# Kernel tuning notes

Measured on AMD Instinct MI355X. Metric: run time of the kernel, lower is better.

## Reference

```python
import jax, jax.numpy as jnp
import numpy as np
from jax import lax

B, L, N_INP, N_HID = 128, 128, 1, 2048
DT = 0.042
RHO = 0.99
INPUT_SCALING = 1.0
GAMMA_MIN, GAMMA_MAX = 2.0, 3.0
EPS_MIN, EPS_MAX = 4.0, 5.0
THETA = 0.1
ALPHA, BETA, TAU_REF = 0.3, 0.4, 0.25  # bio_cell constants


def setup_inputs() -> dict:
    rng = np.random.default_rng(0)
    x = jnp.asarray(rng.standard_normal((B, L, N_INP)), dtype=jnp.float32)
    # per-neuron gamma / epsilon drawn uniformly from (min, max) as in __init__
    gamma = jnp.asarray(rng.uniform(GAMMA_MIN, GAMMA_MAX, N_HID), dtype=jnp.float32)
    epsilon = jnp.asarray(rng.uniform(EPS_MIN, EPS_MAX, N_HID), dtype=jnp.float32)
    # h2h = 2 * (2*rand - 1), then spectral-norm scaled to radius rho
    h2h_np = 2.0 * (2.0 * rng.random((N_HID, N_HID)) - 1.0)
    eig_max = np.abs(np.linalg.eigvals(h2h_np)).max()
    h2h = jnp.asarray(h2h_np * (RHO / eig_max), dtype=jnp.float32)
    x2h = jnp.asarray(rng.random((N_INP, N_HID)) * INPUT_SCALING, dtype=jnp.float32)
    bias = jnp.asarray((rng.random(N_HID) * 2.0 - 1.0) * INPUT_SCALING, dtype=jnp.float32)
    return {"x": x, "h2h": h2h, "x2h": x2h, "bias": bias, "gamma": gamma, "epsilon": epsilon}


def reference(x, h2h, x2h, bias, gamma, epsilon):
    # bio_cell recurrence over L steps; returns mean spike rates (B, N_HID)
    dt = jnp.float32(DT)
    ref_decay = jnp.exp(jnp.float32(-DT / TAU_REF))

    def step(carry, xt):
        hy, hz, ref = carry  # each (B, N_HID); xt: (B, N_INP)
        pre = jnp.tanh(xt @ x2h + hy @ h2h + bias)
        hz = hz + dt * (pre - gamma * hy - epsilon * hz)
        hy = hy + dt * hz
        s = (hy - THETA - ref > 0).astype(hy.dtype)  # spike (non-diff)
        hy = hy * (1.0 - s * ALPHA)
        hz = hz * (1.0 - s * BETA)
        ref = ref * ref_decay + s
        return (hy, hz, ref), s

    z = jnp.zeros((x.shape[0], h2h.shape[0]), x.dtype)
    _, spikes = lax.scan(step, (z, z, z), jnp.swapaxes(x, 0, 1))  # spikes: (L, B, N_HID)
    return spikes.mean(axis=0)
```

## Files before the change

### kernel.cpp

```cpp
#include <hip/hip_runtime.h>
#include <hip/hip_bf16.h>
#include <cmath>

constexpr int   BB  = 128;
constexpr int   LL  = 128;
constexpr int   NH  = 2048;
constexpr int   KD  = 2048;
constexpr int   KQ  = 8;
constexpr float DTc   = 0.042f;
constexpr float THETAc= 0.1f;
constexpr float ALPHAc= 0.3f;
constexpr float BETAc = 0.4f;
constexpr size_t S = (size_t)BB * NH;

typedef float f32x4 __attribute__((ext_vector_type(4)));
typedef short s16x8 __attribute__((ext_vector_type(8)));

__device__ inline ushort f2bf(float f) {
    union { __hip_bfloat16 h; ushort u; } v; v.h = __float2bfloat16(f); return v.u;
}
__device__ inline float bf2f(ushort u) {
    union { ushort u; __hip_bfloat16 h; } v; v.u = u; return __bfloat162float(v.h);
}
__device__ inline void split3(float f, ushort& b1, ushort& b2, ushort& b3) {
    b1 = f2bf(f);  float r  = f - bf2f(b1);
    b2 = f2bf(r);  float r2 = r - bf2f(b2);
    b3 = f2bf(r2);
}

__global__ __launch_bounds__(256) void packB_kernel(
    const float* __restrict__ W, ushort* __restrict__ B1,
    ushort* __restrict__ B2, ushort* __restrict__ B3)
{
    const int gw   = blockIdx.x * 4 + (threadIdx.x >> 6);
    const int lane = threadIdx.x & 63;
    const int kt = gw >> 7;
    const int nb = gw & 127;
    const size_t ob = ((size_t)(kt * 128 + nb) * 64 + lane) * 8;
    const int k0 = kt * 32 + (lane >> 4) * 8;
    const int n  = nb * 16 + (lane & 15);
    #pragma unroll
    for (int e = 0; e < 8; ++e) {
        float w = W[(size_t)(k0 + e) * NH + n];
        ushort x1, x2, x3; split3(w, x1, x2, x3);
        B1[ob + e] = x1; B2[ob + e] = x2; B3[ob + e] = x3;
    }
}

__global__ __launch_bounds__(512) void gemm_mfma(
    const ushort* __restrict__ A1, const ushort* __restrict__ A2,
    const ushort* __restrict__ A3, const ushort* __restrict__ B1,
    const ushort* __restrict__ B2, const ushort* __restrict__ B3,
    float* __restrict__ P)
{
    __shared__ ushort Bs[49152];
    const int tid  = threadIdx.x;
    const int lane = tid & 63;
    const int w    = tid >> 6;
    const int wm   = w >> 1;
    const int wn   = w & 1;
    const int g    = lane >> 4;
    const int r16  = lane & 15;
    const int bx   = blockIdx.x;
    const int kq   = blockIdx.y;
    const int ktb  = kq * 8;

    {
        const size_t gb = ((size_t)((ktb + w) * 128 + bx * 4)) * 512 + (size_t)lane * 8;
        const int lb0 = w * 6144;
        #pragma unroll
        for (int nb = 0; nb < 4; ++nb) {
            __builtin_amdgcn_global_load_lds(B1 + gb + nb * 512, &Bs[lb0 +        nb * 512], 16, 0, 0);
            __builtin_amdgcn_global_load_lds(B2 + gb + nb * 512, &Bs[lb0 + 2048 + nb * 512], 16, 0, 0);
            __builtin_amdgcn_global_load_lds(B3 + gb + nb * 512, &Bs[lb0 + 4096 + nb * 512], 16, 0, 0);
        }
    }

    const size_t aoff = (size_t)(g * 128 + wm * 32 + r16) * 8;

    s16x8 ac[6], an[6];
    #define LDA(kt, d)  do { \
        const size_t ab_ = aoff + (size_t)(ktb + (kt)) * 4096; \
        d[0] = *(const s16x8*)(A1 + ab_);  d[1] = *(const s16x8*)(A1 + ab_ + 128); \
        d[2] = *(const s16x8*)(A2 + ab_);  d[3] = *(const s16x8*)(A2 + ab_ + 128); \
        d[4] = *(const s16x8*)(A3 + ab_);  d[5] = *(const s16x8*)(A3 + ab_ + 128); \
    } while (0)

    f32x4 acc[2][2] = {};

    LDA(0, ac);
    __syncthreads();

    #pragma unroll
    for (int kt = 0; kt < 8; ++kt) {
        if (kt < 7) LDA(kt + 1, an);
        const int lb = kt * 6144 + wn * 1024 + lane * 8;
        s16x8 b1[2], b2[2], b3[2];
        b1[0] = *(const s16x8*)(&Bs[lb]);        b1[1] = *(const s16x8*)(&Bs[lb + 512]);
        b2[0] = *(const s16x8*)(&Bs[lb + 2048]); b2[1] = *(const s16x8*)(&Bs[lb + 2048 + 512]);
        b3[0] = *(const s16x8*)(&Bs[lb + 4096]); b3[1] = *(const s16x8*)(&Bs[lb + 4096 + 512]);

        #pragma unroll
        for (int mf = 0; mf < 2; ++mf)
        #pragma unroll
        for (int nf = 0; nf < 2; ++nf) {
            f32x4 c = acc[mf][nf];
            c = __builtin_amdgcn_mfma_f32_16x16x32_bf16(ac[0 + mf], b1[nf], c, 0, 0, 0);
            c = __builtin_amdgcn_mfma_f32_16x16x32_bf16(ac[0 + mf], b2[nf], c, 0, 0, 0);
            c = __builtin_amdgcn_mfma_f32_16x16x32_bf16(ac[2 + mf], b1[nf], c, 0, 0, 0);
            c = __builtin_amdgcn_mfma_f32_16x16x32_bf16(ac[0 + mf], b3[nf], c, 0, 0, 0);
            c = __builtin_amdgcn_mfma_f32_16x16x32_bf16(ac[2 + mf], b2[nf], c, 0, 0, 0);
            c = __builtin_amdgcn_mfma_f32_16x16x32_bf16(ac[4 + mf], b1[nf], c, 0, 0, 0);
            acc[mf][nf] = c;
        }
        #pragma unroll
        for (int i = 0; i < 6; ++i) ac[i] = an[i];
    }
    #undef LDA

    float* Pp = P + (size_t)kq * S;
    #pragma unroll
    for (int mf = 0; mf < 2; ++mf)
    #pragma unroll
    for (int nf = 0; nf < 2; ++nf) {
        const int col = bx * 64 + wn * 32 + nf * 16 + r16;
        #pragma unroll
        for (int r = 0; r < 4; ++r) {
            const int row = wm * 32 + mf * 16 + g * 4 + r;
            Pp[(size_t)row * NH + col] = acc[mf][nf][r];
        }
    }
}

__global__ __launch_bounds__(256) void update_mfma(
    const float* __restrict__ P, float* __restrict__ hy,
    float* __restrict__ hz, float* __restrict__ refb, float* __restrict__ ssum,
    ushort* __restrict__ A1, ushort* __restrict__ A2, ushort* __restrict__ A3,
    const float* __restrict__ x2h, const float* __restrict__ bias,
    const float* __restrict__ gamma, const float* __restrict__ eps,
    const float* __restrict__ x, int t)
{
    const int i = blockIdx.x * 256 + threadIdx.x;
    const int b = i >> 11;
    const int n = i & (NH - 1);

    float acc = 0.f;
    #pragma unroll
    for (int q = 0; q < KQ; ++q) acc += P[(size_t)q * S + i];

    const float xt = x[(size_t)b * LL + t];
    float pre = tanhf(acc + xt * x2h[n] + bias[n]);

    float hyv = hy[i];
    float hzv = hz[i];
    float rf  = refb[i];
    const float rd = expf(-DTc / 0.25f);

    hzv += DTc * (pre - gamma[n] * hyv - eps[n] * hzv);
    hyv += DTc * hzv;
    float s = (hyv - THETAc - rf > 0.f) ? 1.f : 0.f;
    hyv *= 1.f - s * ALPHAc;
    hzv *= 1.f - s * BETAc;
    rf = rf * rd + s;

    hy[i]   = hyv;
    hz[i]   = hzv;
    refb[i] = rf;
    ssum[i] += s;

    const int kt = n >> 5, gg = (n >> 3) & 3, e = n & 7;
    const size_t o = ((size_t)(kt * 4 + gg) * 128 + b) * 8 + e;
    ushort u1, u2, u3; split3(hyv, u1, u2, u3);
    A1[o] = u1; A2[o] = u2; A3[o] = u3;
}

__global__ __launch_bounds__(512) void finish_kernel(const float* __restrict__ ssum,
                                                     float* __restrict__ out)
{
    const int i = blockIdx.x * 512 + threadIdx.x;
    out[i] = ssum[i] * (1.0f / (float)LL);
}

template<int KCH>
__global__ __launch_bounds__(512) void gemm_vec(
    const float* __restrict__ hy_in, float* __restrict__ P,
    const float* __restrict__ W)
{
    const int lane = threadIdx.x & 63;
    const int w    = __builtin_amdgcn_readfirstlane((int)(threadIdx.x >> 6));
    const int n        = blockIdx.x * 64 + lane;
    const int rowbase  = blockIdx.y * 64 + w * 8;
    const int kq       = blockIdx.z;
    const int k0       = kq * KCH;
    const float* __restrict__ hp = hy_in + (size_t)rowbase * KD + k0;
    const float* __restrict__ Wp = W + (size_t)k0 * NH + n;
    float acc[8] = {0.f,0.f,0.f,0.f,0.f,0.f,0.f,0.f};
    float wc[8], w1[8], w2[8];
    #pragma unroll
    for (int i = 0; i < 8; ++i) w1[i] = Wp[(size_t)i * NH];
    {
        const float* Wq = Wp + (size_t)8 * NH;
        #pragma unroll
        for (int i = 0; i < 8; ++i) w2[i] = Wq[(size_t)i * NH];
    }
    for (int k = 0; k < KCH; k += 8) {
        #pragma unroll
        for (int i = 0; i < 8; ++i) wc[i] = w1[i];
        #pragma unroll
        for (int i = 0; i < 8; ++i) w1[i] = w2[i];
        if (k + 16 < KCH) {
            const float* Wq = Wp + (size_t)(k + 16) * NH;
            #pragma unroll
            for (int i = 0; i < 8; ++i) w2[i] = Wq[(size_t)i * NH];
        }
        #pragma unroll
        for (int j = 0; j < 8; ++j) {
            const float* hr = hp + (size_t)j * KD + k;
            float4 a = *(const float4*)(hr);
            float4 bq = *(const float4*)(hr + 4);
            acc[j] = fmaf(a.x, wc[0], acc[j]);  acc[j] = fmaf(a.y, wc[1], acc[j]);
            acc[j] = fmaf(a.z, wc[2], acc[j]);  acc[j] = fmaf(a.w, wc[3], acc[j]);
            acc[j] = fmaf(bq.x, wc[4], acc[j]); acc[j] = fmaf(bq.y, wc[5], acc[j]);
            acc[j] = fmaf(bq.z, wc[6], acc[j]); acc[j] = fmaf(bq.w, wc[7], acc[j]);
        }
    }
    float* Pp = P + ((size_t)kq * BB + rowbase) * NH + n;
    #pragma unroll
    for (int j = 0; j < 8; ++j) Pp[(size_t)j * NH] = acc[j];
}

__global__ __launch_bounds__(256) void update_vec(
    const float* __restrict__ P, int kqn, const float* __restrict__ hy_in,
    float* __restrict__ hy_out, float* __restrict__ hz,
    float* __restrict__ refb, float* __restrict__ ssum,
    const float* __restrict__ x2h, const float* __restrict__ bias,
    const float* __restrict__ gamma, const float* __restrict__ eps,
    const float* __restrict__ x, int t)
{
    const int i = blockIdx.x * 256 + threadIdx.x;
    const int b = i >> 11;
    const int n = i & (NH - 1);
    float acc = 0.f;
    for (int q = 0; q < kqn; ++q) acc += P[(size_t)q * S + i];
    const float xt = x[(size_t)b * LL + t];
    float pre = tanhf(acc + xt * x2h[n] + bias[n]);
    float hyv = hy_in[i];
    float hzv = hz[i];
    float rf  = refb[i];
    const float rd = expf(-DTc / 0.25f);
    hzv += DTc * (pre - gamma[n] * hyv - eps[n] * hzv);
    hyv += DTc * hzv;
    float s = (hyv - THETAc - rf > 0.f) ? 1.f : 0.f;
    hyv *= 1.f - s * ALPHAc;
    hzv *= 1.f - s * BETAc;
    rf = rf * rd + s;
    hy_out[i] = hyv; hz[i] = hzv; refb[i] = rf; ssum[i] += s;
}

extern "C" void kernel_launch(void* const* d_in, const int* in_sizes, int n_in,
                              void* d_out, int out_size, void* d_ws, size_t ws_size,
                              hipStream_t stream) {
    const float* x     = (const float*)d_in[0];
    const float* W     = (const float*)d_in[1];
    const float* x2h   = (const float*)d_in[2];
    const float* bias  = (const float*)d_in[3];
    const float* gamma = (const float*)d_in[4];
    const float* eps   = (const float*)d_in[5];
    float* out = (float*)d_out;

    const size_t SB = S * sizeof(float);

    const size_t offA   = 4 * SB;
    const size_t offP   = offA + 3 * S * 2;
    const size_t offB   = offP + (size_t)KQ * SB;
    const size_t need   = offB + 3 * (16 * S) * 2;

    if (ws_size >= need) {
        char* base = (char*)d_ws;
        float*  hy = (float*)(base);
        float*  hz = (float*)(base + SB);
        float*  rf = (float*)(base + 2 * SB);
        float*  ss = (float*)(base + 3 * SB);
        ushort* A1 = (ushort*)(base + offA);
        ushort* A2 = A1 + S;
        ushort* A3 = A2 + S;
        float*  P  = (float*)(base + offP);
        ushort* B1 = (ushort*)(base + offB);
        ushort* B2 = B1 + 16 * S;
        ushort* B3 = B2 + 16 * S;

        hipMemsetAsync(d_ws, 0, offP, stream);

        packB_kernel<<<2048, 256, 0, stream>>>(W, B1, B2, B3);

        dim3 ggrid(NH / 64, KQ);
        for (int t = 0; t < LL; ++t) {
            gemm_mfma<<<ggrid, 512, 0, stream>>>(A1, A2, A3, B1, B2, B3, P);
            update_mfma<<<(unsigned)(S / 256), 256, 0, stream>>>(
                P, hy, hz, rf, ss, A1, A2, A3, x2h, bias, gamma, eps, x, t);
        }
        finish_kernel<<<(unsigned)(S / 512), 512, 0, stream>>>(ss, out);
    } else {
        float* ws = (float*)d_ws;
        float* hyA = ws;
        float* hz  = ws + S;
        float* rf  = ws + 2 * S;
        float* ss  = ws + 3 * S;
        float* hyB = ws + 4 * S;
        float* P   = ws + 5 * S;
        const int kq = (ws_size >= 13 * SB) ? 8 : 4;
        hipMemsetAsync(d_ws, 0, 4 * SB, stream);
        dim3 ggrid(NH / 64, BB / 64, kq);
        const float* hin = hyA;
        float* hout = hyB;
        for (int t = 0; t < LL; ++t) {
            if (kq == 8)
                gemm_vec<KD / 8><<<ggrid, 512, 0, stream>>>(hin, P, W);
            else
                gemm_vec<KD / 4><<<ggrid, 512, 0, stream>>>(hin, P, W);
            update_vec<<<(unsigned)(S / 256), 256, 0, stream>>>(
                P, kq, hin, hout, hz, rf, ss, x2h, bias, gamma, eps, x, t);
            const float* tmp = hout; hout = (float*)hin; hin = tmp;
        }
        finish_kernel<<<(unsigned)(S / 512), 512, 0, stream>>>(ss, out);
    }
}
```

Baseline: 2.127 ms.

## Fuse recurrent GEMM and state update into one per-step kernel

Replaces the per-step split-K GEMM kernel plus separate update kernel with a single fused kernel. Each block of 8 waves computes a 32x32 output tile with each wave covering one K-eighth, reduces the partials through LDS, then applies the neuron update and writes the split-bf16 activations into a double-buffered A array. This removes the global partial-sum buffer round trip and one launch per step. In exchange the LDS staging of B is gone, so every block reads its B tiles straight from global memory, and only 256 blocks are launched.

```diff
diff --git a/kernel.cpp b/kernel.cpp
--- a/kernel.cpp
+++ b/kernel.cpp
@@ -6,7 +6,6 @@
 constexpr int   LL  = 128;
 constexpr int   NH  = 2048;
 constexpr int   KD  = 2048;
-constexpr int   KQ  = 8;
 constexpr float DTc   = 0.042f;
 constexpr float THETAc= 0.1f;
 constexpr float ALPHAc= 0.3f;
@@ -47,131 +46,134 @@
     }
 }
 
-__global__ __launch_bounds__(512) void gemm_mfma(
-    const ushort* __restrict__ A1, const ushort* __restrict__ A2,
-    const ushort* __restrict__ A3, const ushort* __restrict__ B1,
-    const ushort* __restrict__ B2, const ushort* __restrict__ B3,
-    float* __restrict__ P)
-{
-    __shared__ ushort Bs[49152];
+__global__ __launch_bounds__(512) void step_fused(
+    const ushort* __restrict__ Ai1, const ushort* __restrict__ Ai2,
+    const ushort* __restrict__ Ai3, ushort* __restrict__ Ao1,
+    ushort* __restrict__ Ao2, ushort* __restrict__ Ao3,
+    const ushort* __restrict__ B1, const ushort* __restrict__ B2,
+    const ushort* __restrict__ B3,
+    float* __restrict__ hy, float* __restrict__ hz,
+    float* __restrict__ refb, float* __restrict__ ssum,
+    const float* __restrict__ x, const float* __restrict__ x2h,
+    const float* __restrict__ bias, const float* __restrict__ gamma,
+    const float* __restrict__ eps, int t)
+{
+    __shared__ float Pred[8][32 * 34];
     const int tid  = threadIdx.x;
     const int lane = tid & 63;
     const int w    = tid >> 6;
-    const int wm   = w >> 1;
-    const int wn   = w & 1;
     const int g    = lane >> 4;
     const int r16  = lane & 15;
-    const int bx   = blockIdx.x;
-    const int kq   = blockIdx.y;
-    const int ktb  = kq * 8;
+    const int bid  = blockIdx.x;
+    const int mb   = bid >> 6;
+    const int c    = bid & 63;
+    const int ktb  = w * 8;
+
+    f32x4 acc[2][2] = {};
+    const size_t aoff = (size_t)(g * 128 + mb * 32 + r16) * 8;
+    const size_t boff = (size_t)(c * 128 + lane) * 8;
+
+    #pragma unroll
+    for (int j = 0; j < 8; ++j) {
+        const int kt = ktb + j;
+        const size_t ab = aoff + (size_t)kt * 4096;
+        const size_t bb = boff + (size_t)kt * 65536;
+        s16x8 a1[2], a2[2], a3[2], b1[2], b2[2], b3[2];
+        #pragma unroll
+        for (int mf = 0; mf < 2; ++mf) {
+            a1[mf] = *(const s16x8*)(Ai1 + ab + mf * 128);
+            a2[mf] = *(const s16x8*)(Ai2 + ab + mf * 128);
+            a3[mf] = *(const s16x8*)(Ai3 + ab + mf * 128);
+        }
+        #pragma unroll
+        for (int nf = 0; nf < 2; ++nf) {
+            b1[nf] = *(const s16x8*)(B1 + bb + nf * 512);
+            b2[nf] = *(const s16x8*)(B2 + bb + nf * 512);
+            b3[nf] = *(const s16x8*)(B3 + bb + nf * 512);
+        }
+        #pragma unroll
+        for (int mf = 0; mf < 2; ++mf)
+        #pragma unroll
+        for (int nf = 0; nf < 2; ++nf) {
+            f32x4 cc = acc[mf][nf];
+            cc = __builtin_amdgcn_mfma_f32_16x16x32_bf16(a1[mf], b1[nf], cc, 0, 0, 0);
+            cc = __builtin_amdgcn_mfma_f32_16x16x32_bf16(a1[mf], b2[nf], cc, 0, 0, 0);
+            cc = __builtin_amdgcn_mfma_f32_16x16x32_bf16(a2[mf], b1[nf], cc, 0, 0, 0);
+            cc = __builtin_amdgcn_mfma_f32_16x16x32_bf16(a1[mf], b3[nf], cc, 0, 0, 0);
+            cc = __builtin_amdgcn_mfma_f32_16x16x32_bf16(a2[mf], b2[nf], cc, 0, 0, 0);
+            cc = __builtin_amdgcn_mfma_f32_16x16x32_bf16(a3[mf], b1[nf], cc, 0, 0, 0);
+            acc[mf][nf] = cc;
+        }
+    }
+
+    #pragma unroll
+    for (int mf = 0; mf < 2; ++mf)
+    #pragma unroll
+    for (int nf = 0; nf < 2; ++nf)
+    #pragma unroll
+    for (int r = 0; r < 4; ++r)
+        Pred[w][(mf * 16 + g * 4 + r) * 34 + nf * 16 + r16] = acc[mf][nf][r];
+
+    __syncthreads();
+
+    const int e0  = tid * 2;
+    const int row = e0 >> 5;
+    const int col = e0 & 31;
+    const int b   = mb * 32 + row;
+    const int n0  = c * 32 + col, n1 = n0 + 1;
+
+    float pa0 = 0.f, pa1 = 0.f;
+    #pragma unroll
+    for (int q = 0; q < 8; ++q) {
+        const float2 pv = *(const float2*)&Pred[q][row * 34 + col];
+        pa0 += pv.x; pa1 += pv.y;
+    }
+
+    const size_t ig = (size_t)b * NH + n0;
+    const float xt = x[(size_t)b * LL + t];
+    const float rd = expf(-DTc / 0.25f);
+    const float2 x2hv = *(const float2*)(x2h + n0);
+    const float2 biv  = *(const float2*)(bias + n0);
+    const float2 gav  = *(const float2*)(gamma + n0);
+    const float2 epv  = *(const float2*)(eps + n0);
+    float2 hyv = *(float2*)(hy + ig);
+    float2 hzv = *(float2*)(hz + ig);
+    float2 rfv = *(float2*)(refb + ig);
+    float2 ssv = *(float2*)(ssum + ig);
 
     {
-        const size_t gb = ((size_t)((ktb + w) * 128 + bx * 4)) * 512 + (size_t)lane * 8;
-        const int lb0 = w * 6144;
-        #pragma unroll
-        for (int nb = 0; nb < 4; ++nb) {
-            __builtin_amdgcn_global_load_lds(B1 + gb + nb * 512, &Bs[lb0 +        nb * 512], 16, 0, 0);
-            __builtin_amdgcn_global_load_lds(B2 + gb + nb * 512, &Bs[lb0 + 2048 + nb * 512], 16, 0, 0);
-            __builtin_amdgcn_global_load_lds(B3 + gb + nb * 512, &Bs[lb0 + 4096 + nb * 512], 16, 0, 0);
-        }
-    }
-
-    const size_t aoff = (size_t)(g * 128 + wm * 32 + r16) * 8;
-
-    s16x8 ac[6], an[6];
-    #define LDA(kt, d)  do { \
-        const size_t ab_ = aoff + (size_t)(ktb + (kt)) * 4096; \
-        d[0] = *(const s16x8*)(A1 + ab_);  d[1] = *(const s16x8*)(A1 + ab_ + 128); \
-        d[2] = *(const s16x8*)(A2 + ab_);  d[3] = *(const s16x8*)(A2 + ab_ + 128); \
-        d[4] = *(const s16x8*)(A3 + ab_);  d[5] = *(const s16x8*)(A3 + ab_ + 128); \
-    } while (0)
-
-    f32x4 acc[2][2] = {};
-
-    LDA(0, ac);
-    __syncthreads();
-
-    #pragma unroll
-    for (int kt = 0; kt < 8; ++kt) {
-        if (kt < 7) LDA(kt + 1, an);
-        const int lb = kt * 6144 + wn * 1024 + lane * 8;
-        s16x8 b1[2], b2[2], b3[2];
-        b1[0] = *(const s16x8*)(&Bs[lb]);        b1[1] = *(const s16x8*)(&Bs[lb + 512]);
-        b2[0] = *(const s16x8*)(&Bs[lb + 2048]); b2[1] = *(const s16x8*)(&Bs[lb + 2048 + 512]);
-        b3[0] = *(const s16x8*)(&Bs[lb + 4096]); b3[1] = *(const s16x8*)(&Bs[lb + 4096 + 512]);
-
-        #pragma unroll
-        for (int mf = 0; mf < 2; ++mf)
-        #pragma unroll
-        for (int nf = 0; nf < 2; ++nf) {
-            f32x4 c = acc[mf][nf];
-            c = __builtin_amdgcn_mfma_f32_16x16x32_bf16(ac[0 + mf], b1[nf], c, 0, 0, 0);
-            c = __builtin_amdgcn_mfma_f32_16x16x32_bf16(ac[0 + mf], b2[nf], c, 0, 0, 0);
-            c = __builtin_amdgcn_mfma_f32_16x16x32_bf16(ac[2 + mf], b1[nf], c, 0, 0, 0);
-            c = __builtin_amdgcn_mfma_f32_16x16x32_bf16(ac[0 + mf], b3[nf], c, 0, 0, 0);
-            c = __builtin_amdgcn_mfma_f32_16x16x32_bf16(ac[2 + mf], b2[nf], c, 0, 0, 0);
-            c = __builtin_amdgcn_mfma_f32_16x16x32_bf16(ac[4 + mf], b1[nf], c, 0, 0, 0);
-            acc[mf][nf] = c;
-        }
-        #pragma unroll
-        for (int i = 0; i < 6; ++i) ac[i] = an[i];
-    }
-    #undef LDA
-
-    float* Pp = P + (size_t)kq * S;
-    #pragma unroll
-    for (int mf = 0; mf < 2; ++mf)
-    #pragma unroll
-    for (int nf = 0; nf < 2; ++nf) {
-        const int col = bx * 64 + wn * 32 + nf * 16 + r16;
-        #pragma unroll
-        for (int r = 0; r < 4; ++r) {
-            const int row = wm * 32 + mf * 16 + g * 4 + r;
-            Pp[(size_t)row * NH + col] = acc[mf][nf][r];
-        }
-    }
-}
-
-__global__ __launch_bounds__(256) void update_mfma(
-    const float* __restrict__ P, float* __restrict__ hy,
-    float* __restrict__ hz, float* __restrict__ refb, float* __restrict__ ssum,
-    ushort* __restrict__ A1, ushort* __restrict__ A2, ushort* __restrict__ A3,
-    const float* __restrict__ x2h, const float* __restrict__ bias,
-    const float* __restrict__ gamma, const float* __restrict__ eps,
-    const float* __restrict__ x, int t)
-{
-    const int i = blockIdx.x * 256 + threadIdx.x;
-    const int b = i >> 11;
-    const int n = i & (NH - 1);
-
-    float acc = 0.f;
-    #pragma unroll
-    for (int q = 0; q < KQ; ++q) acc += P[(size_t)q * S + i];
-
-    const float xt = x[(size_t)b * LL + t];
-    float pre = tanhf(acc + xt * x2h[n] + bias[n]);
-
-    float hyv = hy[i];
-    float hzv = hz[i];
-    float rf  = refb[i];
-    const float rd = expf(-DTc / 0.25f);
-
-    hzv += DTc * (pre - gamma[n] * hyv - eps[n] * hzv);
-    hyv += DTc * hzv;
-    float s = (hyv - THETAc - rf > 0.f) ? 1.f : 0.f;
-    hyv *= 1.f - s * ALPHAc;
-    hzv *= 1.f - s * BETAc;
-    rf = rf * rd + s;
-
-    hy[i]   = hyv;
-    hz[i]   = hzv;
-    refb[i] = rf;
-    ssum[i] += s;
-
-    const int kt = n >> 5, gg = (n >> 3) & 3, e = n & 7;
-    const size_t o = ((size_t)(kt * 4 + gg) * 128 + b) * 8 + e;
-    ushort u1, u2, u3; split3(hyv, u1, u2, u3);
-    A1[o] = u1; A2[o] = u2; A3[o] = u3;
+        float pre = tanhf(pa0 + xt * x2hv.x + biv.x);
+        hzv.x += DTc * (pre - gav.x * hyv.x - epv.x * hzv.x);
+        hyv.x += DTc * hzv.x;
+        float s = (hyv.x - THETAc - rfv.x > 0.f) ? 1.f : 0.f;
+        hyv.x *= 1.f - s * ALPHAc;
+        hzv.x *= 1.f - s * BETAc;
+        rfv.x = rfv.x * rd + s;
+        ssv.x += s;
+        ushort u1, u2, u3; split3(hyv.x, u1, u2, u3);
+        const int kt0 = n0 >> 5, gg = (n0 >> 3) & 3, ee = n0 & 7;
+        const size_t o = ((size_t)(kt0 * 4 + gg) * 128 + b) * 8 + ee;
+        Ao1[o] = u1; Ao2[o] = u2; Ao3[o] = u3;
+    }
+    {
+        float pre = tanhf(pa1 + xt * x2hv.y + biv.y);
+        hzv.y += DTc * (pre - gav.y * hyv.y - epv.y * hzv.y);
+        hyv.y += DTc * hzv.y;
+        float s = (hyv.y - THETAc - rfv.y > 0.f) ? 1.f : 0.f;
+        hyv.y *= 1.f - s * ALPHAc;
+        hzv.y *= 1.f - s * BETAc;
+        rfv.y = rfv.y * rd + s;
+        ssv.y += s;
+        ushort u1, u2, u3; split3(hyv.y, u1, u2, u3);
+        const int kt1 = n1 >> 5, gg = (n1 >> 3) & 3, ee = n1 & 7;
+        const size_t o = ((size_t)(kt1 * 4 + gg) * 128 + b) * 8 + ee;
+        Ao1[o] = u1; Ao2[o] = u2; Ao3[o] = u3;
+    }
+
+    *(float2*)(hy + ig)   = hyv;
+    *(float2*)(hz + ig)   = hzv;
+    *(float2*)(refb + ig) = rfv;
+    *(float2*)(ssum + ig) = ssv;
 }
 
 __global__ __launch_bounds__(512) void finish_kernel(const float* __restrict__ ssum,
@@ -270,34 +272,40 @@
 
     const size_t SB = S * sizeof(float);
 
-    const size_t offA   = 4 * SB;
-    const size_t offP   = offA + 3 * S * 2;
-    const size_t offB   = offP + (size_t)KQ * SB;
+    const size_t offSt  = 3 * S * 2;
+    const size_t offAb  = offSt + 4 * SB;
+    const size_t offB   = offAb + 3 * S * 2;
     const size_t need   = offB + 3 * (16 * S) * 2;
 
     if (ws_size >= need) {
         char* base = (char*)d_ws;
-        float*  hy = (float*)(base);
-        float*  hz = (float*)(base + SB);
-        float*  rf = (float*)(base + 2 * SB);
-        float*  ss = (float*)(base + 3 * SB);
-        ushort* A1 = (ushort*)(base + offA);
-        ushort* A2 = A1 + S;
-        ushort* A3 = A2 + S;
-        float*  P  = (float*)(base + offP);
+        ushort* Aa1 = (ushort*)base;
+        ushort* Aa2 = Aa1 + S;
+        ushort* Aa3 = Aa2 + S;
+        float*  hy = (float*)(base + offSt);
+        float*  hz = hy + S;
+        float*  rf = hz + S;
+        float*  ss = rf + S;
+        ushort* Ab1 = (ushort*)(base + offAb);
+        ushort* Ab2 = Ab1 + S;
+        ushort* Ab3 = Ab2 + S;
         ushort* B1 = (ushort*)(base + offB);
         ushort* B2 = B1 + 16 * S;
         ushort* B3 = B2 + 16 * S;
 
-        hipMemsetAsync(d_ws, 0, offP, stream);
+        hipMemsetAsync(d_ws, 0, offAb, stream);
 
         packB_kernel<<<2048, 256, 0, stream>>>(W, B1, B2, B3);
 
-        dim3 ggrid(NH / 64, KQ);
+        ushort *i1 = Aa1, *i2 = Aa2, *i3 = Aa3, *o1 = Ab1, *o2 = Ab2, *o3 = Ab3;
         for (int t = 0; t < LL; ++t) {
-            gemm_mfma<<<ggrid, 512, 0, stream>>>(A1, A2, A3, B1, B2, B3, P);
-            update_mfma<<<(unsigned)(S / 256), 256, 0, stream>>>(
-                P, hy, hz, rf, ss, A1, A2, A3, x2h, bias, gamma, eps, x, t);
+            step_fused<<<256, 512, 0, stream>>>(i1, i2, i3, o1, o2, o3,
+                                                B1, B2, B3, hy, hz, rf, ss,
+                                                x, x2h, bias, gamma, eps, t);
+            ushort* tp;
+            tp = i1; i1 = o1; o1 = tp;
+            tp = i2; i2 = o2; o2 = tp;
+            tp = i3; i3 = o3; o3 = tp;
         }
         finish_kernel<<<(unsigned)(S / 512), 512, 0, stream>>>(ss, out);
     } else {
```

Result: faster. 1.799 ms (-15.4%).
